# Optimization experiments

Hardware: AMD Instinct MI355X
Metric: run time of the kernel (lower is better)

Reference implementation:

```python
import jax, jax.numpy as jnp
import numpy as np
import itertools

DIM, KEY_DIM, H, ATTN_RATIO = 576, 32, 18, 4
RES = (14, 14)
DV = ATTN_RATIO * KEY_DIM  # 128
DH = DV * H                # 2304
NH_KD = KEY_DIM * H        # 576
LN_EPS = 1e-5


def _build_bias_idxs():
    points = list(itertools.product(range(RES[0]), range(RES[1])))
    N = len(points)
    offsets = {}
    idxs = []
    for p1 in points:
        for p2 in points:
            off = (abs(p1[0] - p2[0]), abs(p1[1] - p2[1]))
            offsets.setdefault(off, len(offsets))
            idxs.append(offsets[off])
    return np.array(idxs, dtype=np.int64).reshape(N, N), len(offsets)


def setup_inputs() -> dict:
    key = jax.random.key(0)
    ks = jax.random.split(key, 8)
    B, N = 128, RES[0] * RES[1]
    idxs_np, n_off = _build_bias_idxs()  # [N,N], 196 offsets
    x = jax.random.normal(ks[0], (B, N, DIM), dtype=jnp.float32)
    ln_g = jnp.ones((DIM,), jnp.float32)
    ln_b = jnp.zeros((DIM,), jnp.float32)
    qkv_w = jax.random.normal(ks[1], (DH + 2 * NH_KD, DIM), jnp.float32) * (DIM ** -0.5)
    qkv_b = jnp.zeros((DH + 2 * NH_KD,), jnp.float32)
    proj_w = jax.random.normal(ks[2], (DIM, DH), jnp.float32) * (DH ** -0.5)
    proj_b = jnp.zeros((DIM,), jnp.float32)
    attn_biases = jax.random.normal(ks[3], (H, n_off), jnp.float32) * 0.02
    bias_idxs = jnp.asarray(idxs_np)
    return {"x": x, "ln_g": ln_g, "ln_b": ln_b, "qkv_w": qkv_w, "qkv_b": qkv_b,
            "proj_w": proj_w, "proj_b": proj_b, "attn_biases": attn_biases,
            "bias_idxs": bias_idxs}


def reference(x, ln_g, ln_b, qkv_w, qkv_b, proj_w, proj_b, attn_biases, bias_idxs):
    B, N, C = x.shape
    scale = KEY_DIM ** -0.5
    # LayerNorm
    mu = jnp.mean(x, axis=-1, keepdims=True)
    var = jnp.mean(jnp.square(x - mu), axis=-1, keepdims=True)
    xn = (x - mu) * jax.lax.rsqrt(var + LN_EPS) * ln_g + ln_b
    # QKV
    qkv = xn @ qkv_w.T + qkv_b                      # [B,N,H*(2*KD+DV)]
    qkv = qkv.reshape(B, N, H, 2 * KEY_DIM + DV)
    q = qkv[..., :KEY_DIM]                          # [B,N,H,KD]
    k = qkv[..., KEY_DIM:2 * KEY_DIM]
    v = qkv[..., 2 * KEY_DIM:]                      # [B,N,H,DV]
    # Scores + gathered relative-position bias
    bias = attn_biases[:, bias_idxs]                # [H,N,N]
    attn = jnp.einsum('bnhk,bmhk->bhnm', q, k) * scale + bias
    attn = jax.nn.softmax(attn, axis=-1)
    out = jnp.einsum('bhnm,bmhd->bnhd', attn, v).reshape(B, N, DH)
    return out @ proj_w.T + proj_b
```

## Files before the change

kernel.cpp:

```cpp
#include <hip/hip_runtime.h>
#include <hip/hip_bf16.h>
#include <cstdint>


typedef uint32_t u32;
typedef unsigned short u16;
using f32x4 = __attribute__((ext_vector_type(4))) float;
using s16x8 = __attribute__((ext_vector_type(8))) short;

#define DEVFN static __device__ __forceinline__

DEVFN u16 f2bf(float f) {
  u32 u = __builtin_bit_cast(u32, f);
  u = (u + 0x7fffu + ((u >> 16) & 1u)) >> 16;
  return (u16)u;
}

DEVFN u32 cvtpk_bf16(float lo, float hi) {
  u32 r;
  asm("v_cvt_pk_bf16_f32 %0, %1, %2" : "=v"(r) : "v"(lo), "v"(hi));
  return r;
}

DEVFN float exp2_fast(float x) {
  float r;
  asm("v_exp_f32 %0, %1" : "=v"(r) : "v"(x));
  return r;
}

DEVFN void gload_lds16(const void* g, void* l) {
  typedef const __attribute__((address_space(1))) uint32_t* gp_t;
  typedef __attribute__((address_space(3))) uint32_t* lp_t;
  __builtin_amdgcn_global_load_lds((gp_t)g, (lp_t)l, 16, 0, 0);
}

__global__ void k_cvt(const float* __restrict__ in, u16* __restrict__ out, int n) {
  int i = blockIdx.x * 256 + threadIdx.x;
  if (i < n) out[i] = f2bf(in[i]);
}

__global__ void k_cvt_pad(const float* __restrict__ in, u16* __restrict__ out) {
  int i = blockIdx.x * 256 + threadIdx.x;
  int r = i / 2304, c = i % 2304;
  out[i] = (r < 576) ? f2bf(in[r * 2304 + c]) : (u16)0;
}

__global__ void k_bias(const float* __restrict__ biases, const int* __restrict__ idxs,
                       float* __restrict__ out, int noff) {
  int i = blockIdx.x * 256 + threadIdx.x;
  int r = i & 3, g = (i >> 2) & 3, q16 = (i >> 4) & 15;
  int t = i >> 8;
  int mt = t % 13, t2 = t / 13;
  int qt = t2 % 13, h = t2 / 13;
  int q = qt * 16 + q16, m = mt * 16 + g * 4 + r;
  float v = -1e30f;
  if (q < 196 && m < 196)
    v = biases[h * noff + idxs[q * 196 + m]] * 1.4426950408889634f;
  out[i] = v;
}

__launch_bounds__(256)
__global__ void k_ln(const float* __restrict__ x, const float* __restrict__ g,
                     const float* __restrict__ b, u16* __restrict__ xn) {
  int t = blockIdx.x * 4 + (threadIdx.x >> 6);
  int l = threadIdx.x & 63;
  const float* xt = x + (size_t)t * 576;
  const float4* x4 = (const float4*)xt;
  float4 v0 = x4[l], v1 = x4[64 + l];
  float v2 = xt[512 + l];
  float s = v0.x + v0.y + v0.z + v0.w + v1.x + v1.y + v1.z + v1.w + v2;
  float q = v0.x * v0.x + v0.y * v0.y + v0.z * v0.z + v0.w * v0.w +
            v1.x * v1.x + v1.y * v1.y + v1.z * v1.z + v1.w * v1.w + v2 * v2;
  for (int o = 1; o < 64; o <<= 1) {
    s += __shfl_xor(s, o, 64);
    q += __shfl_xor(q, o, 64);
  }
  float mean = s * (1.f / 576.f);
  float var = q * (1.f / 576.f) - mean * mean;
  float rstd = rsqrtf(var + 1e-5f);
  const float4* g4 = (const float4*)g;
  const float4* b4 = (const float4*)b;
  float4 ga = g4[l], gb = g4[64 + l];
  float4 ba = b4[l], bb = b4[64 + l];
  float gc = g[512 + l], bc = b[512 + l];
  u16* ot = xn + (size_t)t * 576;
  ushort4 o0, o1;
  o0.x = f2bf((v0.x - mean) * rstd * ga.x + ba.x);
  o0.y = f2bf((v0.y - mean) * rstd * ga.y + ba.y);
  o0.z = f2bf((v0.z - mean) * rstd * ga.z + ba.z);
  o0.w = f2bf((v0.w - mean) * rstd * ga.w + ba.w);
  o1.x = f2bf((v1.x - mean) * rstd * gb.x + bb.x);
  o1.y = f2bf((v1.y - mean) * rstd * gb.y + bb.y);
  o1.z = f2bf((v1.z - mean) * rstd * gb.z + bb.z);
  o1.w = f2bf((v1.w - mean) * rstd * gb.w + bb.w);
  ((ushort4*)ot)[l] = o0;
  ((ushort4*)ot)[64 + l] = o1;
  ot[512 + l] = f2bf((v2 - mean) * rstd * gc + bc);
}

template <bool OBF, int AMODE>
__launch_bounds__(512, 2)
__global__ void k_gemm(const u16* __restrict__ A, const u16* __restrict__ Bt,
                       const float* __restrict__ bias, void* __restrict__ C,
                       int K, int nvalid) {
  __shared__ u16 As[3][256 * 32];
  __shared__ u16 Bs[3][128 * 32];
  const int tid = threadIdx.x, lane = tid & 63, w = tid >> 6;
  const int wr = w >> 1, wc = w & 1;
  const int l15 = lane & 15, g = lane >> 4;
  const int nwg = gridDim.x * gridDim.y;
  int wgid = blockIdx.x + gridDim.x * blockIdx.y;
  int xcd = wgid & 7, local = wgid >> 3;
  int nq = nwg >> 3, rr = nwg & 7;
  int id2 = ((xcd < rr) ? xcd * (nq + 1) : rr * (nq + 1) + (xcd - rr) * nq) + local;
  const size_t m0 = (size_t)(id2 / gridDim.x) * 256;
  const size_t n0 = (size_t)(id2 % gridDim.x) * 128;
  const int Kb = K * 2;
  const int KbA = (AMODE == 0) ? K * 2 : 6912;
  const char* Ab = (const char*)A + m0 * KbA;
  const char* Bb = (const char*)Bt + n0 * Kb;
  f32x4 acc[4][4] = {};

  auto stage = [&](int buf, int kt) {
    const int abase = (AMODE == 0) ? kt * 2 : ((kt >> 7) * 384 + 128 + ((kt & 127) << 1));
#pragma unroll
    for (int j = 0; j < 2; ++j) {
      int c = j * 512 + tid;
      int r = c >> 2, sp = c & 3;
      int sl = sp ^ ((r >> 1) & 3);
      gload_lds16(Ab + (size_t)r * KbA + abase + sl * 16,
                  (char*)As + buf * 16384 + c * 16);
    }
    {
      int c = tid;
      int r = c >> 2, sp = c & 3;
      int sl = sp ^ ((r >> 1) & 3);
      gload_lds16(Bb + (size_t)r * Kb + kt * 2 + sl * 16,
                  (char*)Bs + buf * 8192 + c * 16);
    }
  };

  const int NT = K >> 5;
  stage(0, 0);
  stage(1, 32);
  asm volatile("s_waitcnt vmcnt(3)" ::: "memory");
  __builtin_amdgcn_sched_barrier(0);
  __builtin_amdgcn_s_barrier();

  int br = 0, bs = 2;
  for (int t = 0; t < NT; ++t) {
    const char* AsB = (const char*)As + br * 16384;
    const char* BsB = (const char*)Bs + br * 8192;
    s16x8 af[4], bfr[4];
#pragma unroll
    for (int i = 0; i < 4; ++i) {
      int ra = wr * 64 + i * 16 + l15;
      af[i] = *(const s16x8*)(AsB + ra * 64 + ((g ^ ((ra >> 1) & 3)) << 4));
      int rb = wc * 64 + i * 16 + l15;
      bfr[i] = *(const s16x8*)(BsB + rb * 64 + ((g ^ ((rb >> 1) & 3)) << 4));
    }
    if (t + 2 < NT) stage(bs, (t + 2) * 32);
#pragma unroll
    for (int mi = 0; mi < 4; ++mi)
#pragma unroll
      for (int ni = 0; ni < 4; ++ni)
        acc[mi][ni] = __builtin_amdgcn_mfma_f32_16x16x32_bf16(af[mi], bfr[ni], acc[mi][ni], 0, 0, 0);
    if (t + 1 < NT) {
      if (t + 2 < NT) {
        asm volatile("s_waitcnt vmcnt(3)" ::: "memory");
      } else {
        asm volatile("s_waitcnt vmcnt(0)" ::: "memory");
      }
      __builtin_amdgcn_sched_barrier(0);
      __builtin_amdgcn_s_barrier();
    }
    br = (br == 2) ? 0 : br + 1;
    bs = (bs == 2) ? 0 : bs + 1;
  }

#pragma unroll
  for (int ni = 0; ni < 4; ++ni) {
    int n = (int)n0 + wc * 64 + ni * 16 + l15;
    if (n >= nvalid) continue;
    float bv = bias[n];
#pragma unroll
    for (int mi = 0; mi < 4; ++mi) {
      size_t m = m0 + wr * 64 + mi * 16 + ((lane >> 4) << 2);
#pragma unroll
      for (int r = 0; r < 4; ++r) {
        float val = acc[mi][ni][r] + bv;
        if (OBF)
          ((u16*)C)[(m + r) * (size_t)nvalid + n] = f2bf(val);
        else
          ((float*)C)[(m + r) * (size_t)nvalid + n] = val;
      }
    }
  }
}

__launch_bounds__(512, 2)
__global__ void k_attn(u16* __restrict__ qkv, const float* __restrict__ biasf) {
  constexpr int LDV = 234;
  __shared__ u16 Vl[128 * LDV];
  __shared__ u16 Kl[13 * 64 * 8];
  const int h = blockIdx.x, b = blockIdx.y;
  const int tid = threadIdx.x, lane = tid & 63, w = tid >> 6;
  const int g = lane >> 4, q16 = lane & 15;
  const size_t tok0 = (size_t)b * 196;
  u16* qkvb = qkv + tok0 * 3456 + (size_t)h * 192;

  {
    int c = tid;
    int tok = min((c >> 6) * 16 + (c & 15), 195);
    gload_lds16(qkvb + (size_t)tok * 3456 + 32 + ((c >> 4) & 3) * 8,
                (char*)Kl + (size_t)(w * 64) * 16);
    if (tid < 320) {
      int c2 = 512 + tid;
      int tok2 = min((c2 >> 6) * 16 + (c2 & 15), 195);
      gload_lds16(qkvb + (size_t)tok2 * 3456 + 32 + ((c2 >> 4) & 3) * 8,
                  (char*)Kl + (size_t)(512 + w * 64) * 16);
    }
  }
  {
    int l15 = lane & 15, g2 = lane >> 4;
    for (int j = w; j < 56; j += 8) {
      int db = j / 14, mb = j % 14;
      int m = mb * 16 + l15, d8 = db * 4 + g2;
      int mc = min(m, 195);
      s16x8 v = *(const s16x8*)(qkvb + (size_t)mc * 3456 + 64 + d8 * 8);
#pragma unroll
      for (int e = 0; e < 8; ++e) Vl[(d8 * 8 + e) * LDV + m] = (u16)v[e];
    }
  }
  __syncthreads();

  const float scale = 0.17677669529663687f * 1.4426950408889634f;
  for (int qt = w; qt < 13; qt += 8) {
    int q = qt * 16 + q16;
    s16x8 qf = *(const s16x8*)(qkvb + (size_t)min(q, 195) * 3456 + g * 8);
    const float* bq = biasf + (((size_t)(h * 13 + qt) * 13) << 8) + (q16 << 4) + (g << 2);
    f32x4 acc[8] = {};
    float sum = 0.f;
    const int L1 = ((g & 1) << 5) + q16;
    const int L2 = L1 + 16;
    const bool hiSel = (g >> 1) != 0;
#pragma unroll
    for (int kk = 0; kk < 7; ++kk) {
      u32 a0, a1, b0 = 0u, b1 = 0u;
      {
        s16x8 kf = *(const s16x8*)(Kl + ((size_t)(2 * kk) * 64 + lane) * 8);
        f32x4 z = {};
        f32x4 t = __builtin_amdgcn_mfma_f32_16x16x32_bf16(kf, qf, z, 0, 0, 0);
        f32x4 b4 = *(const f32x4*)(bq + (2 * kk) * 256);
        float e0 = exp2_fast(t[0] * scale + b4[0]);
        float e1 = exp2_fast(t[1] * scale + b4[1]);
        float e2 = exp2_fast(t[2] * scale + b4[2]);
        float e3 = exp2_fast(t[3] * scale + b4[3]);
        sum += (e0 + e1) + (e2 + e3);
        a0 = cvtpk_bf16(e0, e1);
        a1 = cvtpk_bf16(e2, e3);
      }
      if (2 * kk + 1 < 13) {
        s16x8 kf = *(const s16x8*)(Kl + ((size_t)(2 * kk + 1) * 64 + lane) * 8);
        f32x4 z = {};
        f32x4 t = __builtin_amdgcn_mfma_f32_16x16x32_bf16(kf, qf, z, 0, 0, 0);
        f32x4 b4 = *(const f32x4*)(bq + (2 * kk + 1) * 256);
        float e0 = exp2_fast(t[0] * scale + b4[0]);
        float e1 = exp2_fast(t[1] * scale + b4[1]);
        float e2 = exp2_fast(t[2] * scale + b4[2]);
        float e3 = exp2_fast(t[3] * scale + b4[3]);
        sum += (e0 + e1) + (e2 + e3);
        b0 = cvtpk_bf16(e0, e1);
        b1 = cvtpk_bf16(e2, e3);
      }
      u32 rA0 = __shfl((int)a0, L1, 64), rA1 = __shfl((int)a1, L1, 64);
      u32 rA2 = __shfl((int)a0, L2, 64), rA3 = __shfl((int)a1, L2, 64);
      u32 rB0 = __shfl((int)b0, L1, 64), rB1 = __shfl((int)b1, L1, 64);
      u32 rB2 = __shfl((int)b0, L2, 64), rB3 = __shfl((int)b1, L2, 64);
      union {
        u32 u[4];
        s16x8 v;
      } pa;
      pa.u[0] = hiSel ? rB0 : rA0;
      pa.u[1] = hiSel ? rB1 : rA1;
      pa.u[2] = hiSel ? rB2 : rA2;
      pa.u[3] = hiSel ? rB3 : rA3;
#pragma unroll
      for (int dt = 0; dt < 8; ++dt) {
        s16x8 vf = *(const s16x8*)(Vl + (size_t)(dt * 16 + q16) * LDV + kk * 32 + g * 8);
        acc[dt] = __builtin_amdgcn_mfma_f32_16x16x32_bf16(pa.v, vf, acc[dt], 0, 0, 0);
      }
    }
    sum += __shfl_xor(sum, 16, 64);
    sum += __shfl_xor(sum, 32, 64);
    float inv[4];
#pragma unroll
    for (int r = 0; r < 4; ++r) inv[r] = 1.f / __shfl(sum, g * 4 + r, 64);
#pragma unroll
    for (int dp = 0; dp < 4; ++dp) {
#pragma unroll
      for (int r = 0; r < 4; ++r) {
        int qq = qt * 16 + g * 4 + r;
        if (qq < 196) {
          u32 pk = cvtpk_bf16(acc[2 * dp][r] * inv[r], acc[2 * dp + 1][r] * inv[r]);
          u16* op = qkvb + (size_t)qq * 3456 + 64 + dp * 32 + q16;
          op[0] = (u16)pk;
          op[16] = (u16)(pk >> 16);
        }
      }
    }
  }
}

extern "C" void kernel_launch(void* const* d_in, const int* in_sizes, int n_in,
                              void* d_out, int out_size, void* d_ws, size_t ws_size,
                              hipStream_t stream) {
  const float* x = (const float*)d_in[0];
  const float* ln_g = (const float*)d_in[1];
  const float* ln_b = (const float*)d_in[2];
  const float* qkv_w = (const float*)d_in[3];
  const float* qkv_b = (const float*)d_in[4];
  const float* proj_w = (const float*)d_in[5];
  const float* proj_b = (const float*)d_in[6];
  const float* attnb = (const float*)d_in[7];
  const int* idxs = (const int*)d_in[8];
  const int noff = in_sizes[7] / 18;

  char* ws = (char*)d_ws;
  u16* qkv = (u16*)(ws);
  u16* wq = (u16*)(ws + 173408256);
  u16* wp = (u16*)(ws + 177389568);
  float* bfull = (float*)(ws + 180338688);
  const size_t need = 183453696;
  if (ws_size < need) return;

  u16* xn = (u16*)d_out;
  float* out = (float*)d_out;

  k_cvt<<<7776, 256, 0, stream>>>(qkv_w, wq, 1990656);
  k_cvt_pad<<<5760, 256, 0, stream>>>(proj_w, wp);
  k_bias<<<3042, 256, 0, stream>>>(attnb, idxs, bfull, noff);
  k_ln<<<6272, 256, 0, stream>>>(x, ln_g, ln_b, xn);
  k_gemm<true, 0><<<dim3(27, 98), 512, 0, stream>>>(xn, wq, qkv_b, qkv, 576, 3456);
  k_attn<<<dim3(18, 128), 512, 0, stream>>>(qkv, bfull);
  k_gemm<false, 1><<<dim3(5, 98), 512, 0, stream>>>(qkv, wp, proj_b, out, 2304, 576);
}
```

Measured before the change: 359.2 us.

## Stage GEMM epilogue through LDS for coalesced stores and merge prep kernels

```diff
diff --git a/kernel.cpp b/kernel.cpp
--- a/kernel.cpp
+++ b/kernel.cpp
@@ -34,29 +34,30 @@
   __builtin_amdgcn_global_load_lds((gp_t)g, (lp_t)l, 16, 0, 0);
 }
 
-__global__ void k_cvt(const float* __restrict__ in, u16* __restrict__ out, int n) {
-  int i = blockIdx.x * 256 + threadIdx.x;
-  if (i < n) out[i] = f2bf(in[i]);
-}
-
-__global__ void k_cvt_pad(const float* __restrict__ in, u16* __restrict__ out) {
-  int i = blockIdx.x * 256 + threadIdx.x;
-  int r = i / 2304, c = i % 2304;
-  out[i] = (r < 576) ? f2bf(in[r * 2304 + c]) : (u16)0;
-}
-
-__global__ void k_bias(const float* __restrict__ biases, const int* __restrict__ idxs,
-                       float* __restrict__ out, int noff) {
-  int i = blockIdx.x * 256 + threadIdx.x;
-  int r = i & 3, g = (i >> 2) & 3, q16 = (i >> 4) & 15;
-  int t = i >> 8;
-  int mt = t % 13, t2 = t / 13;
-  int qt = t2 % 13, h = t2 / 13;
-  int q = qt * 16 + q16, m = mt * 16 + g * 4 + r;
-  float v = -1e30f;
-  if (q < 196 && m < 196)
-    v = biases[h * noff + idxs[q * 196 + m]] * 1.4426950408889634f;
-  out[i] = v;
+__global__ void k_prep(const float* __restrict__ qkv_w, const float* __restrict__ proj_w,
+                       const float* __restrict__ biases, const int* __restrict__ idxs,
+                       u16* __restrict__ wq, u16* __restrict__ wp,
+                       float* __restrict__ bfull, int noff) {
+  int bid = blockIdx.x;
+  if (bid < 7776) {
+    int i = bid * 256 + threadIdx.x;
+    if (i < 1990656) wq[i] = f2bf(qkv_w[i]);
+  } else if (bid < 7776 + 5760) {
+    int i = (bid - 7776) * 256 + threadIdx.x;
+    int r = i / 2304, c = i % 2304;
+    wp[i] = (r < 576) ? f2bf(proj_w[r * 2304 + c]) : (u16)0;
+  } else {
+    int i = (bid - 7776 - 5760) * 256 + threadIdx.x;
+    int r = i & 3, g = (i >> 2) & 3, q16 = (i >> 4) & 15;
+    int t = i >> 8;
+    int mt = t % 13, t2 = t / 13;
+    int qt = t2 % 13, h = t2 / 13;
+    int q = qt * 16 + q16, m = mt * 16 + g * 4 + r;
+    float v = -1e30f;
+    if (q < 196 && m < 196)
+      v = biases[h * noff + idxs[q * 196 + m]] * 1.4426950408889634f;
+    bfull[i] = v;
+  }
 }
 
 __launch_bounds__(256)
@@ -103,8 +104,9 @@
 __global__ void k_gemm(const u16* __restrict__ A, const u16* __restrict__ Bt,
                        const float* __restrict__ bias, void* __restrict__ C,
                        int K, int nvalid) {
-  __shared__ u16 As[3][256 * 32];
-  __shared__ u16 Bs[3][128 * 32];
+  __shared__ char smem[73728];
+  char* AsB0 = smem;
+  char* BsB0 = smem + 49152;
   const int tid = threadIdx.x, lane = tid & 63, w = tid >> 6;
   const int wr = w >> 1, wc = w & 1;
   const int l15 = lane & 15, g = lane >> 4;
@@ -129,14 +131,14 @@
       int r = c >> 2, sp = c & 3;
       int sl = sp ^ ((r >> 1) & 3);
       gload_lds16(Ab + (size_t)r * KbA + abase + sl * 16,
-                  (char*)As + buf * 16384 + c * 16);
+                  AsB0 + buf * 16384 + c * 16);
     }
     {
       int c = tid;
       int r = c >> 2, sp = c & 3;
       int sl = sp ^ ((r >> 1) & 3);
       gload_lds16(Bb + (size_t)r * Kb + kt * 2 + sl * 16,
-                  (char*)Bs + buf * 8192 + c * 16);
+                  BsB0 + buf * 8192 + c * 16);
     }
   };
 
@@ -149,8 +151,8 @@
 
   int br = 0, bs = 2;
   for (int t = 0; t < NT; ++t) {
-    const char* AsB = (const char*)As + br * 16384;
-    const char* BsB = (const char*)Bs + br * 8192;
+    const char* AsB = AsB0 + br * 16384;
+    const char* BsB = BsB0 + br * 8192;
     s16x8 af[4], bfr[4];
 #pragma unroll
     for (int i = 0; i < 4; ++i) {
@@ -178,22 +180,61 @@
     bs = (bs == 2) ? 0 : bs + 1;
   }
 
-#pragma unroll
-  for (int ni = 0; ni < 4; ++ni) {
-    int n = (int)n0 + wc * 64 + ni * 16 + l15;
-    if (n >= nvalid) continue;
-    float bv = bias[n];
-#pragma unroll
-    for (int mi = 0; mi < 4; ++mi) {
-      size_t m = m0 + wr * 64 + mi * 16 + ((lane >> 4) << 2);
-#pragma unroll
-      for (int r = 0; r < 4; ++r) {
-        float val = acc[mi][ni][r] + bv;
-        if (OBF)
-          ((u16*)C)[(m + r) * (size_t)nvalid + n] = f2bf(val);
-        else
-          ((float*)C)[(m + r) * (size_t)nvalid + n] = val;
-      }
+  __syncthreads();
+  if (OBF) {
+    u16* Cs = (u16*)smem;
+#pragma unroll
+    for (int ni = 0; ni < 4; ++ni) {
+      int n_loc = wc * 64 + ni * 16 + l15;
+      float bv = bias[n0 + n_loc];
+#pragma unroll
+      for (int mi = 0; mi < 4; ++mi) {
+        int m_base = wr * 64 + mi * 16 + g * 4;
+#pragma unroll
+        for (int r = 0; r < 4; ++r)
+          Cs[(m_base + r) * 128 + n_loc] = f2bf(acc[mi][ni][r] + bv);
+      }
+    }
+    __syncthreads();
+    u16* Cg = (u16*)C + m0 * (size_t)nvalid + n0;
+#pragma unroll
+    for (int i = 0; i < 8; ++i) {
+      int c = i * 512 + tid;
+      int row = c >> 4, col8 = (c & 15) * 8;
+      s16x8 v = *(const s16x8*)(Cs + row * 128 + col8);
+      *(s16x8*)(Cg + (size_t)row * nvalid + col8) = v;
+    }
+  } else {
+    float* Cs = (float*)smem;
+#pragma unroll
+    for (int h = 0; h < 2; ++h) {
+      if (wc == h) {
+#pragma unroll
+        for (int ni = 0; ni < 4; ++ni) {
+          int n_loc = ni * 16 + l15;
+          int n_glob = (int)n0 + h * 64 + n_loc;
+          float bv = (n_glob < nvalid) ? bias[n_glob] : 0.f;
+#pragma unroll
+          for (int mi = 0; mi < 4; ++mi) {
+            int m_base = wr * 64 + mi * 16 + g * 4;
+#pragma unroll
+            for (int r = 0; r < 4; ++r)
+              Cs[(m_base + r) * 64 + n_loc] = acc[mi][ni][r] + bv;
+          }
+        }
+      }
+      __syncthreads();
+#pragma unroll
+      for (int i = 0; i < 8; ++i) {
+        int c = i * 512 + tid;
+        int row = c >> 4, col4 = (c & 15) * 4;
+        int n_glob = (int)n0 + h * 64 + col4;
+        if (n_glob < nvalid) {
+          float4 v = *(const float4*)(Cs + row * 64 + col4);
+          *(float4*)((float*)C + (size_t)(m0 + row) * nvalid + n_glob) = v;
+        }
+      }
+      if (h == 0) __syncthreads();
     }
   }
 }
@@ -337,9 +378,7 @@
   u16* xn = (u16*)d_out;
   float* out = (float*)d_out;
 
-  k_cvt<<<7776, 256, 0, stream>>>(qkv_w, wq, 1990656);
-  k_cvt_pad<<<5760, 256, 0, stream>>>(proj_w, wp);
-  k_bias<<<3042, 256, 0, stream>>>(attnb, idxs, bfull, noff);
+  k_prep<<<16578, 256, 0, stream>>>(qkv_w, proj_w, attnb, idxs, wq, wp, bfull, noff);
   k_ln<<<6272, 256, 0, stream>>>(x, ln_g, ln_b, xn);
   k_gemm<true, 0><<<dim3(27, 98), 512, 0, stream>>>(xn, wq, qkv_b, qkv, 576, 3456);
   k_attn<<<dim3(18, 128), 512, 0, stream>>>(qkv, bfull);
```

After: 344.9 us. -4.0%, faster.
